# Performance work log

Hardware: AMD Instinct MI355X
Metric: run time of the kernel (lower is better)

Reference implementation:

```python
import jax, jax.numpy as jnp
import numpy as np

BATCH = 4096
DIM = 128
TEMP = 0.5

def setup_inputs() -> dict:
    key = jax.random.key(0)
    k1, k2 = jax.random.split(key)
    proj_1 = jax.random.normal(k1, (BATCH, DIM), dtype=jnp.float32)
    proj_2 = jax.random.normal(k2, (BATCH, DIM), dtype=jnp.float32)
    return {"proj_1": proj_1, "proj_2": proj_2}

def _l2norm(x, eps=1e-12):
    # matches F.normalize(p=2, dim=1)
    n = jnp.sqrt(jnp.sum(x * x, axis=1, keepdims=True))
    return x / jnp.maximum(n, eps)

def reference(proj_1, proj_2):
    B = proj_1.shape[0]
    z_i = _l2norm(proj_1)
    z_j = _l2norm(proj_2)
    reps = jnp.concatenate([z_i, z_j], axis=0)          # [2B, D]
    # cosine similarity of normalized vectors == dot product; (2B,D)x(D,2B) matmul
    sim = reps @ reps.T                                 # [2B, 2B]
    sim_ij = jnp.einsum('bd,bd->b', z_i, z_j)           # diag(sim, +B)
    sim_ji = sim_ij                                     # diag(sim, -B) is symmetric
    positives = jnp.concatenate([sim_ij, sim_ji], axis=0)  # [2B]
    nominator = jnp.exp(positives / TEMP)
    mask = (~jnp.eye(2 * B, dtype=bool)).astype(sim.dtype)
    denominator = jnp.sum(mask * jnp.exp(sim / TEMP), axis=1)  # [2B]
    all_losses = -jnp.log(nominator / denominator)
    loss = jnp.sum(all_losses) / (2 * B)
    return loss
```

## Files before the change

kernel.cpp:

```cpp
#include <hip/hip_runtime.h>
#include <hip/hip_bf16.h>
#include <math.h>

#define BATCH 4096
#define DIM 128
#define TWO_B 8192
#define SCALE 1.69864374f

typedef float floatx4 __attribute__((ext_vector_type(4)));
typedef int   intx4  __attribute__((ext_vector_type(4)));
typedef long  longx2 __attribute__((ext_vector_type(2)));

__device__ __forceinline__ longx2 as_l2(intx4 v) {
    union { intx4 a; longx2 b; } u; u.a = v; return u.b;
}
__device__ __forceinline__ unsigned char to_fp8(float v) {
    return (unsigned char)(__builtin_amdgcn_cvt_pk_fp8_f32(v, v, 0, false) & 0xff);
}


__global__ __launch_bounds__(256) void norm_kernel(const float* __restrict__ p1,
                                                   const float* __restrict__ p2,
                                                   unsigned char* __restrict__ repsF,
                                                   float* __restrict__ pos,
                                                   float* __restrict__ denom,
                                                   float* __restrict__ out) {
    int tid = threadIdx.x;
    if (tid < 8) denom[blockIdx.x * 8 + tid] = 0.0f;
    int w = tid >> 6, l = tid & 63;
    int b = blockIdx.x * 4 + w;
    const float* r1 = p1 + (size_t)b * DIM;
    const float* r2 = p2 + (size_t)b * DIM;
    float x0 = r1[l], x1 = r1[l + 64];
    float y0 = r2[l], y1 = r2[l + 64];
    float s1 = x0 * x0 + x1 * x1;
    float s2 = y0 * y0 + y1 * y1;
    float s12 = x0 * y0 + x1 * y1;
    #pragma unroll
    for (int off = 32; off; off >>= 1) {
        s1  += __shfl_xor(s1, off);
        s2  += __shfl_xor(s2, off);
        s12 += __shfl_xor(s12, off);
    }
    float n1 = fmaxf(sqrtf(s1), 1e-12f);
    float n2 = fmaxf(sqrtf(s2), 1e-12f);
    float i1 = SCALE / n1;
    float i2 = SCALE / n2;

    int r1i = b, r2i = b + BATCH;
    int off0 = ((l >> 5) & 1) * 8 + ((l >> 3) & 3) * 256 + (l & 7);
    size_t a1 = (size_t)(r1i >> 4) * 2048 + (r1i & 15) * 16 + off0;
    size_t a2 = (size_t)(r2i >> 4) * 2048 + (r2i & 15) * 16 + off0;
    repsF[a1]        = to_fp8(x0 * i1);
    repsF[a1 + 1024] = to_fp8(x1 * i1);
    repsF[a2]        = to_fp8(y0 * i2);
    repsF[a2 + 1024] = to_fp8(y1 * i2);

    if (l == 0) {
        pos[b] = s12 / (n1 * n2);
        if (b == 0) out[0] = 0.0f;
    }
}

__global__ __launch_bounds__(256, 4) void sim_kernel(const unsigned char* __restrict__ repsF,
                                                     float* __restrict__ denom) {
    __shared__ float lds[4][16][68];
    int tid = threadIdx.x;
    int wid = tid >> 6, lane = tid & 63;
    int wm = wid >> 1, wn = wid & 1;
    int lr = lane & 15, q = lane >> 4;
    int r = blockIdx.y;
    int c = blockIdx.x;
    int TM, TN;
    if (c < 64 - r) { TM = r;      TN = r + c; }
    else            { TM = 63 - r; TN = TM + (c - (64 - r)); }
    if (TM == TN && wm == 1 && wn == 0) return;
    int tm = 2 * TM + wm, tn = 2 * TN + wn;
    bool diag = (tm == tn);

    const char* base = (const char*)repsF;
    int lofs = q * 256 + lr * 16;
    const char* ab = base + tm * 8192 + lofs;
    const char* bb = base + tn * 8192 + lofs;

    longx2 aF[4][2], bF[4][2];
    #pragma unroll
    for (int mi = 0; mi < 4; ++mi)
        #pragma unroll
        for (int h = 0; h < 2; ++h) {
            aF[mi][h] = as_l2(*(const intx4*)(ab + mi * 2048 + h * 1024));
            bF[mi][h] = as_l2(*(const intx4*)(bb + mi * 2048 + h * 1024));
        }

    float cs[4] = {0.0f, 0.0f, 0.0f, 0.0f};
    floatx4 rpacc[4];

    #pragma unroll
    for (int p = 0; p < 2; ++p) {
        floatx4 acc[4][2] = {};
        #pragma unroll
        for (int ck = 0; ck < 4; ++ck) {
            int h = ck >> 1, sel = ck & 1;
            #pragma unroll
            for (int mi = 0; mi < 4; ++mi)
                #pragma unroll
                for (int nn = 0; nn < 2; ++nn)
                    acc[mi][nn] = __builtin_amdgcn_mfma_f32_16x16x32_fp8_fp8(
                        aF[mi][h][sel], bF[2 * p + nn][h][sel], acc[mi][nn], 0, 0, 0);
        }
        #pragma unroll
        for (int mi = 0; mi < 4; ++mi) {
            #pragma unroll
            for (int reg = 0; reg < 4; ++reg) {
                float e0 = __builtin_amdgcn_exp2f(acc[mi][0][reg]);
                float e1 = __builtin_amdgcn_exp2f(acc[mi][1][reg]);
                if (diag && (q * 4 + reg) == lr) {
                    if (mi == 2 * p)     e0 = 0.0f;
                    if (mi == 2 * p + 1) e1 = 0.0f;
                }
                cs[2 * p]     += e0;
                cs[2 * p + 1] += e1;
                float rsum = e0 + e1;
                rpacc[mi][reg] = (p == 0) ? rsum : (rpacc[mi][reg] + rsum);
            }
        }
    }

    float* myl = &lds[wid][0][0];
    #pragma unroll
    for (int mi = 0; mi < 4; ++mi)
        *(floatx4*)&myl[lr * 68 + mi * 16 + q * 4] = rpacc[mi];
    asm volatile("s_waitcnt lgkmcnt(0)" ::: "memory");
    {
        float rs = 0.0f;
        #pragma unroll
        for (int j = 0; j < 16; ++j)
            rs += myl[j * 68 + lane];
        atomicAdd(&denom[tm * 64 + lane], rs);
    }
    if (!diag) {
        #pragma unroll
        for (int ni = 0; ni < 4; ++ni) {
            cs[ni] += __shfl_xor(cs[ni], 16);
            cs[ni] += __shfl_xor(cs[ni], 32);
        }
        if (q == 0) {
            #pragma unroll
            for (int ni = 0; ni < 4; ++ni)
                atomicAdd(&denom[tn * 64 + ni * 16 + lr], cs[ni]);
        }
    }
}

__global__ __launch_bounds__(256) void finish_kernel(const float* __restrict__ denom,
                                                     const float* __restrict__ pos,
                                                     float* __restrict__ out) {
    int r = blockIdx.x * 256 + threadIdx.x;
    float v = __logf(denom[r]) - 2.0f * pos[r & (BATCH - 1)];
    #pragma unroll
    for (int off = 32; off; off >>= 1) v += __shfl_xor(v, off);
    if ((threadIdx.x & 63) == 0) atomicAdd(out, v * (1.0f / TWO_B));
}

extern "C" void kernel_launch(void* const* d_in, const int* in_sizes, int n_in,
                              void* d_out, int out_size, void* d_ws, size_t ws_size,
                              hipStream_t stream) {
    const float* p1 = (const float*)d_in[0];
    const float* p2 = (const float*)d_in[1];
    float* out = (float*)d_out;

    char* ws = (char*)d_ws;
    unsigned char* repsF = (unsigned char*)ws;
    float* pos   = (float*)(ws + (size_t)TWO_B * DIM);
    float* denom = pos + BATCH;

    norm_kernel<<<BATCH / 4, 256, 0, stream>>>(p1, p2, repsF, pos, denom, out);
    sim_kernel<<<dim3(65, 32), 256, 0, stream>>>(repsF, denom);
    finish_kernel<<<TWO_B / 256, 256, 0, stream>>>(denom, pos, out);
}
```

Before: 74.27 us.

## Fuse norm, similarity and finish kernels into one persistent kernel with grid barrier

Replaces the three launches with a single persistent kernel of 512 blocks. Each block normalizes its rows, then waits at a global atomic barrier before looping over the similarity tiles. The last block to finish, found with an atomic ticket, computes the final log-sum reduction. This removes two kernel launches and the gaps between them. In exchange it adds a memset, a spin barrier that assumes all 512 blocks are resident at once, and fewer blocks than the original 2080 tiles, so each block does about four tiles in sequence.

```diff
diff --git a/kernel.cpp b/kernel.cpp
--- a/kernel.cpp
+++ b/kernel.cpp
@@ -1,11 +1,11 @@
 #include <hip/hip_runtime.h>
-#include <hip/hip_bf16.h>
 #include <math.h>
 
 #define BATCH 4096
 #define DIM 128
 #define TWO_B 8192
 #define SCALE 1.69864374f
+#define NBLK 512
 
 typedef float floatx4 __attribute__((ext_vector_type(4)));
 typedef int   intx4  __attribute__((ext_vector_type(4)));
@@ -19,147 +19,179 @@
 }
 
 
-__global__ __launch_bounds__(256) void norm_kernel(const float* __restrict__ p1,
-                                                   const float* __restrict__ p2,
-                                                   unsigned char* __restrict__ repsF,
-                                                   float* __restrict__ pos,
-                                                   float* __restrict__ denom,
-                                                   float* __restrict__ out) {
-    int tid = threadIdx.x;
-    if (tid < 8) denom[blockIdx.x * 8 + tid] = 0.0f;
-    int w = tid >> 6, l = tid & 63;
-    int b = blockIdx.x * 4 + w;
-    const float* r1 = p1 + (size_t)b * DIM;
-    const float* r2 = p2 + (size_t)b * DIM;
-    float x0 = r1[l], x1 = r1[l + 64];
-    float y0 = r2[l], y1 = r2[l + 64];
-    float s1 = x0 * x0 + x1 * x1;
-    float s2 = y0 * y0 + y1 * y1;
-    float s12 = x0 * y0 + x1 * y1;
-    #pragma unroll
-    for (int off = 32; off; off >>= 1) {
-        s1  += __shfl_xor(s1, off);
-        s2  += __shfl_xor(s2, off);
-        s12 += __shfl_xor(s12, off);
-    }
-    float n1 = fmaxf(sqrtf(s1), 1e-12f);
-    float n2 = fmaxf(sqrtf(s2), 1e-12f);
-    float i1 = SCALE / n1;
-    float i2 = SCALE / n2;
-
-    int r1i = b, r2i = b + BATCH;
-    int off0 = ((l >> 5) & 1) * 8 + ((l >> 3) & 3) * 256 + (l & 7);
-    size_t a1 = (size_t)(r1i >> 4) * 2048 + (r1i & 15) * 16 + off0;
-    size_t a2 = (size_t)(r2i >> 4) * 2048 + (r2i & 15) * 16 + off0;
-    repsF[a1]        = to_fp8(x0 * i1);
-    repsF[a1 + 1024] = to_fp8(x1 * i1);
-    repsF[a2]        = to_fp8(y0 * i2);
-    repsF[a2 + 1024] = to_fp8(y1 * i2);
-
-    if (l == 0) {
-        pos[b] = s12 / (n1 * n2);
-        if (b == 0) out[0] = 0.0f;
-    }
-}
-
-__global__ __launch_bounds__(256, 4) void sim_kernel(const unsigned char* __restrict__ repsF,
-                                                     float* __restrict__ denom) {
+__global__ __launch_bounds__(256, 4) void fused_kernel(const float* __restrict__ p1,
+                                                       const float* __restrict__ p2,
+                                                       unsigned char* __restrict__ repsF,
+                                                       float* __restrict__ pos,
+                                                       float* __restrict__ denom,
+                                                       unsigned int* __restrict__ gsync,
+                                                       float* __restrict__ out) {
     __shared__ float lds[4][16][68];
+    __shared__ int lastflag;
+    __shared__ float red[4];
     int tid = threadIdx.x;
     int wid = tid >> 6, lane = tid & 63;
-    int wm = wid >> 1, wn = wid & 1;
-    int lr = lane & 15, q = lane >> 4;
-    int r = blockIdx.y;
-    int c = blockIdx.x;
-    int TM, TN;
-    if (c < 64 - r) { TM = r;      TN = r + c; }
-    else            { TM = 63 - r; TN = TM + (c - (64 - r)); }
-    if (TM == TN && wm == 1 && wn == 0) return;
-    int tm = 2 * TM + wm, tn = 2 * TN + wn;
-    bool diag = (tm == tn);
-
-    const char* base = (const char*)repsF;
-    int lofs = q * 256 + lr * 16;
-    const char* ab = base + tm * 8192 + lofs;
-    const char* bb = base + tn * 8192 + lofs;
-
-    longx2 aF[4][2], bF[4][2];
+
+    if (tid < 16) denom[blockIdx.x * 16 + tid] = 0.0f;
     #pragma unroll
-    for (int mi = 0; mi < 4; ++mi)
+    for (int it = 0; it < 2; ++it) {
+        int b = blockIdx.x * 8 + it * 4 + wid;
+        const float* r1 = p1 + (size_t)b * DIM;
+        const float* r2 = p2 + (size_t)b * DIM;
+        float x0 = r1[lane], x1 = r1[lane + 64];
+        float y0 = r2[lane], y1 = r2[lane + 64];
+        float s1 = x0 * x0 + x1 * x1;
+        float s2 = y0 * y0 + y1 * y1;
+        float s12 = x0 * y0 + x1 * y1;
         #pragma unroll
-        for (int h = 0; h < 2; ++h) {
-            aF[mi][h] = as_l2(*(const intx4*)(ab + mi * 2048 + h * 1024));
-            bF[mi][h] = as_l2(*(const intx4*)(bb + mi * 2048 + h * 1024));
-        }
-
-    float cs[4] = {0.0f, 0.0f, 0.0f, 0.0f};
-    floatx4 rpacc[4];
-
-    #pragma unroll
-    for (int p = 0; p < 2; ++p) {
-        floatx4 acc[4][2] = {};
-        #pragma unroll
-        for (int ck = 0; ck < 4; ++ck) {
-            int h = ck >> 1, sel = ck & 1;
+        for (int off = 32; off; off >>= 1) {
+            s1  += __shfl_xor(s1, off);
+            s2  += __shfl_xor(s2, off);
+            s12 += __shfl_xor(s12, off);
+        }
+        float n1 = fmaxf(sqrtf(s1), 1e-12f);
+        float n2 = fmaxf(sqrtf(s2), 1e-12f);
+        float i1 = SCALE / n1;
+        float i2 = SCALE / n2;
+
+        int r1i = b, r2i = b + BATCH;
+        int off0 = ((lane >> 5) & 1) * 8 + ((lane >> 3) & 3) * 256 + (lane & 7);
+        size_t a1 = (size_t)(r1i >> 4) * 2048 + (r1i & 15) * 16 + off0;
+        size_t a2 = (size_t)(r2i >> 4) * 2048 + (r2i & 15) * 16 + off0;
+        repsF[a1]        = to_fp8(x0 * i1);
+        repsF[a1 + 1024] = to_fp8(x1 * i1);
+        repsF[a2]        = to_fp8(y0 * i2);
+        repsF[a2 + 1024] = to_fp8(y1 * i2);
+
+        if (lane == 0) pos[b] = s12 / (n1 * n2);
+    }
+
+    __syncthreads();
+    if (tid == 0) {
+        __threadfence();
+        atomicAdd(&gsync[0], 1u);
+        int guard = 0;
+        while (__hip_atomic_load(&gsync[0], __ATOMIC_RELAXED,
+                                 __HIP_MEMORY_SCOPE_AGENT) < (unsigned)NBLK &&
+               guard < 2000000) {
+            __builtin_amdgcn_s_sleep(8);
+            ++guard;
+        }
+        __threadfence();
+    }
+    __syncthreads();
+
+    {
+        int wm = wid >> 1, wn = wid & 1;
+        int lr = lane & 15, q = lane >> 4;
+        const char* base = (const char*)repsF;
+        int lofs = q * 256 + lr * 16;
+
+        for (int t = blockIdx.x; t < 65 * 32; t += NBLK) {
+            int r = t / 65;
+            int c = t - r * 65;
+            int TM, TN;
+            if (c < 64 - r) { TM = r;      TN = r + c; }
+            else            { TM = 63 - r; TN = TM + (c - (64 - r)); }
+            if (TM == TN && wm == 1 && wn == 0) continue;
+            int tm = 2 * TM + wm, tn = 2 * TN + wn;
+            bool diag = (tm == tn);
+
+            const char* ab = base + tm * 8192 + lofs;
+            const char* bb = base + tn * 8192 + lofs;
+
+            longx2 aF[4][2], bF[4][2];
             #pragma unroll
             for (int mi = 0; mi < 4; ++mi)
                 #pragma unroll
-                for (int nn = 0; nn < 2; ++nn)
-                    acc[mi][nn] = __builtin_amdgcn_mfma_f32_16x16x32_fp8_fp8(
-                        aF[mi][h][sel], bF[2 * p + nn][h][sel], acc[mi][nn], 0, 0, 0);
-        }
+                for (int h = 0; h < 2; ++h) {
+                    aF[mi][h] = as_l2(*(const intx4*)(ab + mi * 2048 + h * 1024));
+                    bF[mi][h] = as_l2(*(const intx4*)(bb + mi * 2048 + h * 1024));
+                }
+
+            float cs[4] = {0.0f, 0.0f, 0.0f, 0.0f};
+            floatx4 rpacc[4];
+
+            #pragma unroll
+            for (int p = 0; p < 2; ++p) {
+                floatx4 acc[4][2] = {};
+                #pragma unroll
+                for (int ck = 0; ck < 4; ++ck) {
+                    int h = ck >> 1, sel = ck & 1;
+                    #pragma unroll
+                    for (int mi = 0; mi < 4; ++mi)
+                        #pragma unroll
+                        for (int nn = 0; nn < 2; ++nn)
+                            acc[mi][nn] = __builtin_amdgcn_mfma_f32_16x16x32_fp8_fp8(
+                                aF[mi][h][sel], bF[2 * p + nn][h][sel], acc[mi][nn], 0, 0, 0);
+                }
+                #pragma unroll
+                for (int mi = 0; mi < 4; ++mi) {
+                    #pragma unroll
+                    for (int reg = 0; reg < 4; ++reg) {
+                        float e0 = __builtin_amdgcn_exp2f(acc[mi][0][reg]);
+                        float e1 = __builtin_amdgcn_exp2f(acc[mi][1][reg]);
+                        if (diag && (q * 4 + reg) == lr) {
+                            if (mi == 2 * p)     e0 = 0.0f;
+                            if (mi == 2 * p + 1) e1 = 0.0f;
+                        }
+                        cs[2 * p]     += e0;
+                        cs[2 * p + 1] += e1;
+                        float rsum = e0 + e1;
+                        rpacc[mi][reg] = (p == 0) ? rsum : (rpacc[mi][reg] + rsum);
+                    }
+                }
+            }
+
+            float* myl = &lds[wid][0][0];
+            #pragma unroll
+            for (int mi = 0; mi < 4; ++mi)
+                *(floatx4*)&myl[lr * 68 + mi * 16 + q * 4] = rpacc[mi];
+            asm volatile("s_waitcnt lgkmcnt(0)" ::: "memory");
+            {
+                float rs = 0.0f;
+                #pragma unroll
+                for (int j = 0; j < 16; ++j)
+                    rs += myl[j * 68 + lane];
+                atomicAdd(&denom[tm * 64 + lane], rs);
+            }
+            if (!diag) {
+                #pragma unroll
+                for (int ni = 0; ni < 4; ++ni) {
+                    cs[ni] += __shfl_xor(cs[ni], 16);
+                    cs[ni] += __shfl_xor(cs[ni], 32);
+                }
+                if (q == 0) {
+                    #pragma unroll
+                    for (int ni = 0; ni < 4; ++ni)
+                        atomicAdd(&denom[tn * 64 + ni * 16 + lr], cs[ni]);
+                }
+            }
+        }
+    }
+
+    __syncthreads();
+    if (tid == 0) {
+        __threadfence();
+        unsigned int tk = atomicAdd(&gsync[1], 1u);
+        lastflag = (tk == (unsigned)(NBLK - 1));
+    }
+    __syncthreads();
+    if (lastflag) {
+        __threadfence();
+        float v = 0.0f;
         #pragma unroll
-        for (int mi = 0; mi < 4; ++mi) {
-            #pragma unroll
-            for (int reg = 0; reg < 4; ++reg) {
-                float e0 = __builtin_amdgcn_exp2f(acc[mi][0][reg]);
-                float e1 = __builtin_amdgcn_exp2f(acc[mi][1][reg]);
-                if (diag && (q * 4 + reg) == lr) {
-                    if (mi == 2 * p)     e0 = 0.0f;
-                    if (mi == 2 * p + 1) e1 = 0.0f;
-                }
-                cs[2 * p]     += e0;
-                cs[2 * p + 1] += e1;
-                float rsum = e0 + e1;
-                rpacc[mi][reg] = (p == 0) ? rsum : (rpacc[mi][reg] + rsum);
-            }
-        }
-    }
-
-    float* myl = &lds[wid][0][0];
-    #pragma unroll
-    for (int mi = 0; mi < 4; ++mi)
-        *(floatx4*)&myl[lr * 68 + mi * 16 + q * 4] = rpacc[mi];
-    asm volatile("s_waitcnt lgkmcnt(0)" ::: "memory");
-    {
-        float rs = 0.0f;
+        for (int k = 0; k < 32; ++k) {
+            int rr = k * 256 + tid;
+            v += __logf(denom[rr]) - 2.0f * pos[rr & (BATCH - 1)];
+        }
         #pragma unroll
-        for (int j = 0; j < 16; ++j)
-            rs += myl[j * 68 + lane];
-        atomicAdd(&denom[tm * 64 + lane], rs);
-    }
-    if (!diag) {
-        #pragma unroll
-        for (int ni = 0; ni < 4; ++ni) {
-            cs[ni] += __shfl_xor(cs[ni], 16);
-            cs[ni] += __shfl_xor(cs[ni], 32);
-        }
-        if (q == 0) {
-            #pragma unroll
-            for (int ni = 0; ni < 4; ++ni)
-                atomicAdd(&denom[tn * 64 + ni * 16 + lr], cs[ni]);
-        }
-    }
-}
-
-__global__ __launch_bounds__(256) void finish_kernel(const float* __restrict__ denom,
-                                                     const float* __restrict__ pos,
-                                                     float* __restrict__ out) {
-    int r = blockIdx.x * 256 + threadIdx.x;
-    float v = __logf(denom[r]) - 2.0f * pos[r & (BATCH - 1)];
-    #pragma unroll
-    for (int off = 32; off; off >>= 1) v += __shfl_xor(v, off);
-    if ((threadIdx.x & 63) == 0) atomicAdd(out, v * (1.0f / TWO_B));
+        for (int off = 32; off; off >>= 1) v += __shfl_xor(v, off);
+        if (lane == 0) red[wid] = v;
+        __syncthreads();
+        if (tid == 0)
+            out[0] = ((red[0] + red[1]) + (red[2] + red[3])) * (1.0f / TWO_B);
+    }
 }
 
 extern "C" void kernel_launch(void* const* d_in, const int* in_sizes, int n_in,
@@ -173,8 +205,8 @@
     unsigned char* repsF = (unsigned char*)ws;
     float* pos   = (float*)(ws + (size_t)TWO_B * DIM);
     float* denom = pos + BATCH;
-
-    norm_kernel<<<BATCH / 4, 256, 0, stream>>>(p1, p2, repsF, pos, denom, out);
-    sim_kernel<<<dim3(65, 32), 256, 0, stream>>>(repsF, denom);
-    finish_kernel<<<TWO_B / 256, 256, 0, stream>>>(denom, pos, out);
-}
+    unsigned int* gsync = (unsigned int*)(denom + TWO_B);
+
+    hipMemsetAsync(gsync, 0, 2 * sizeof(unsigned int), stream);
+    fused_kernel<<<NBLK, 256, 0, stream>>>(p1, p2, repsF, pos, denom, gsync, out);
+}
```

Measured after the change: 127.6 us. +71.9%, slower.

## Fuse finish into sim kernel via per-tile partials and last-arriver reduction

Applied to the files above, without the earlier changes.

Replaces float atomicAdd accumulation of row denominators with plain stores of per-tile partial sums into a 128x8192 partial buffer. A per-row-tile arrival counter lets the last wave to finish a tile row sum the partials, take the log, and add to the output, so the separate finish kernel launch goes away. This removes contended float atomics and one kernel launch, at the cost of a 4 MB partial buffer, extra counter atomics and a serialized tail reduction by the last arriver.

```diff
diff --git a/kernel.cpp b/kernel.cpp
--- a/kernel.cpp
+++ b/kernel.cpp
@@ -17,16 +17,24 @@
 __device__ __forceinline__ unsigned char to_fp8(float v) {
     return (unsigned char)(__builtin_amdgcn_cvt_pk_fp8_f32(v, v, 0, false) & 0xff);
 }
+template <typename T>
+__device__ __forceinline__ void st_agent(T* p, T v) {
+    __hip_atomic_store(p, v, __ATOMIC_RELAXED, __HIP_MEMORY_SCOPE_AGENT);
+}
+template <typename T>
+__device__ __forceinline__ T ld_agent(const T* p) {
+    return __hip_atomic_load(p, __ATOMIC_RELAXED, __HIP_MEMORY_SCOPE_AGENT);
+}
 
 
 __global__ __launch_bounds__(256) void norm_kernel(const float* __restrict__ p1,
                                                    const float* __restrict__ p2,
                                                    unsigned char* __restrict__ repsF,
                                                    float* __restrict__ pos,
-                                                   float* __restrict__ denom,
+                                                   unsigned int* __restrict__ cnt,
                                                    float* __restrict__ out) {
     int tid = threadIdx.x;
-    if (tid < 8) denom[blockIdx.x * 8 + tid] = 0.0f;
+    if (blockIdx.x == 0 && tid < 128) cnt[tid] = 0u;
     int w = tid >> 6, l = tid & 63;
     int b = blockIdx.x * 4 + w;
     const float* r1 = p1 + (size_t)b * DIM;
@@ -63,7 +71,10 @@
 }
 
 __global__ __launch_bounds__(256, 4) void sim_kernel(const unsigned char* __restrict__ repsF,
-                                                     float* __restrict__ denom) {
+                                                     const float* __restrict__ pos,
+                                                     float* __restrict__ part,
+                                                     unsigned int* __restrict__ cnt,
+                                                     float* __restrict__ out) {
     __shared__ float lds[4][16][68];
     int tid = threadIdx.x;
     int wid = tid >> 6, lane = tid & 63;
@@ -136,7 +147,7 @@
         #pragma unroll
         for (int j = 0; j < 16; ++j)
             rs += myl[j * 68 + lane];
-        atomicAdd(&denom[tm * 64 + lane], rs);
+        st_agent(&part[(size_t)tn * TWO_B + tm * 64 + lane], rs);
     }
     if (!diag) {
         #pragma unroll
@@ -144,22 +155,42 @@
             cs[ni] += __shfl_xor(cs[ni], 16);
             cs[ni] += __shfl_xor(cs[ni], 32);
         }
-        if (q == 0) {
-            #pragma unroll
-            for (int ni = 0; ni < 4; ++ni)
-                atomicAdd(&denom[tn * 64 + ni * 16 + lr], cs[ni]);
-        }
-    }
-}
-
-__global__ __launch_bounds__(256) void finish_kernel(const float* __restrict__ denom,
-                                                     const float* __restrict__ pos,
-                                                     float* __restrict__ out) {
-    int r = blockIdx.x * 256 + threadIdx.x;
-    float v = __logf(denom[r]) - 2.0f * pos[r & (BATCH - 1)];
-    #pragma unroll
-    for (int off = 32; off; off >>= 1) v += __shfl_xor(v, off);
-    if ((threadIdx.x & 63) == 0) atomicAdd(out, v * (1.0f / TWO_B));
+        float cv = (lane & 32) ? ((lane & 16) ? cs[3] : cs[2])
+                               : ((lane & 16) ? cs[1] : cs[0]);
+        st_agent(&part[(size_t)tm * TWO_B + tn * 64 + lane], cv);
+    }
+
+    asm volatile("s_waitcnt vmcnt(0)" ::: "memory");
+    unsigned int tkr = 0u, tkc = 0u;
+    if (lane == 0) {
+        tkr = atomicAdd(&cnt[tm], 1u);
+        if (!diag) tkc = atomicAdd(&cnt[tn], 1u);
+    }
+    tkr = (unsigned)__shfl((int)tkr, 0);
+    tkc = (unsigned)__shfl((int)tkc, 0);
+
+    #pragma unroll
+    for (int which = 0; which < 2; ++which) {
+        unsigned int tk = which ? tkc : tkr;
+        int v = which ? tn : tm;
+        if (tk == 127u && (which == 0 || !diag)) {
+            const float* pk = part + (size_t)v * 64 + lane;
+            float s0 = 0.0f, s1 = 0.0f, s2 = 0.0f, s3 = 0.0f;
+            #pragma unroll
+            for (int k = 0; k < 128; k += 4) {
+                s0 += ld_agent(pk + (size_t)(k + 0) * TWO_B);
+                s1 += ld_agent(pk + (size_t)(k + 1) * TWO_B);
+                s2 += ld_agent(pk + (size_t)(k + 2) * TWO_B);
+                s3 += ld_agent(pk + (size_t)(k + 3) * TWO_B);
+            }
+            int rr = v * 64 + lane;
+            float val = __logf((s0 + s1) + (s2 + s3))
+                      - 2.0f * ld_agent(&pos[rr & (BATCH - 1)]);
+            #pragma unroll
+            for (int off = 32; off; off >>= 1) val += __shfl_xor(val, off);
+            if (lane == 0) atomicAdd(out, val * (1.0f / TWO_B));
+        }
+    }
 }
 
 extern "C" void kernel_launch(void* const* d_in, const int* in_sizes, int n_in,
@@ -172,9 +203,9 @@
     char* ws = (char*)d_ws;
     unsigned char* repsF = (unsigned char*)ws;
     float* pos   = (float*)(ws + (size_t)TWO_B * DIM);
-    float* denom = pos + BATCH;
-
-    norm_kernel<<<BATCH / 4, 256, 0, stream>>>(p1, p2, repsF, pos, denom, out);
-    sim_kernel<<<dim3(65, 32), 256, 0, stream>>>(repsF, denom);
-    finish_kernel<<<TWO_B / 256, 256, 0, stream>>>(denom, pos, out);
-}
+    float* part  = pos + BATCH;
+    unsigned int* cnt = (unsigned int*)(part + (size_t)128 * TWO_B);
+
+    norm_kernel<<<BATCH / 4, 256, 0, stream>>>(p1, p2, repsF, pos, cnt, out);
+    sim_kernel<<<dim3(65, 32), 256, 0, stream>>>(repsF, pos, part, cnt, out);
+}
```

Measured after the change: 129.5 us. 74.4% more time.
